# Kernel tuning notes

Hardware: AMD Instinct MI355X
Metric: run time of the kernel (lower is better)

Reference implementation:

```python
import jax, jax.numpy as jnp
import numpy as np

DIM = 256; HEADS = 8; HD = DIM // HEADS; WIN = 3; LOCAL = WIN * WIN
SR = 8; SHARED = 4; ROUTED = 2
B = 4; RES = 64; TBL = 4096
EPS = 1.1920929e-07  # torch.finfo(float32).eps


def _l2(x):
    return x / jnp.clip(jnp.linalg.norm(x, axis=-1, keepdims=True), EPS)


def _forward(x, relative_coords_table, q_w, q_b, kv_w, kv_b, temperature,
             query_embedding, rpb_local, learnable_tokens, learnable_bias,
             cpb1_w, cpb1_b, cpb2_w, cpb2_b, sr_w, sr_b, norm_g, norm_b,
             wg_w, wg0_w, wg1_w, proj_w, proj_b, relative_pos_index, H, W):
    B_, N, C = x.shape
    pH, pW = H // SR, W // SR
    PL = pH * pW
    _x = x.reshape(B_ * N, C)

    # ---- MoE head routing: top-k gating over routed heads ----
    gates = jax.nn.softmax(_x @ wg_w.T, axis=1)                 # (BN, n_routed)
    _, idx = jax.lax.top_k(gates, ROUTED)
    mask = jax.nn.one_hot(idx, gates.shape[1], dtype=gates.dtype).sum(axis=1)
    rg = gates * mask
    rg = rg / jnp.clip(jnp.sum(rg, axis=1, keepdims=True), EPS)
    routed_gates = rg.reshape(B_, N, -1) * ROUTED

    # ---- seq-length-scale buffer: log(local valid-window count + pool_len) ----
    r = WIN // 2
    ch = np.minimum(np.arange(H) + r, H - 1) - np.maximum(np.arange(H) - r, 0) + 1
    cw = np.minimum(np.arange(W) + r, W - 1) - np.maximum(np.arange(W) - r, 0) + 1
    sls = jnp.asarray(np.log(np.outer(ch, cw).reshape(-1, 1).astype(np.float32) + PL))

    # ---- queries ----
    q = (x @ q_w.T + q_b).reshape(B_, N, HEADS, HD).transpose(0, 2, 1, 3)
    q_norm = _l2(q)                                             # (B,h,N,d)
    q_scaled = (q_norm + query_embedding) * jax.nn.softplus(temperature) * sls

    # ---- local branch: unfold normalized k and v over 3x3 windows (zero pad) ----
    kv = x @ kv_w.T + kv_b                                      # (B,N,2C)
    k_loc = _l2(kv[..., :C].reshape(B_, N, HEADS, HD)).reshape(B_, N, C)
    kvl = jnp.concatenate([k_loc, kv[..., C:]], -1).transpose(0, 2, 1).reshape(B_, 2 * C, H, W)
    kvp = jnp.pad(kvl, ((0, 0), (0, 0), (r, r), (r, r)))
    patches = jnp.stack([kvp[:, :, i:i + H, j:j + W] for i in range(WIN) for j in range(WIN)], axis=2)
    patches = patches.reshape(B_, 2 * HEADS, HD, LOCAL, N).transpose(0, 1, 4, 2, 3)  # (B,2h,N,d,L)
    k_local, v_local = patches[:, :HEADS], patches[:, HEADS:]

    attn_local = jnp.einsum('bhnd,bhndl->bhnl', q_scaled, k_local) + rpb_local[:, None, :]

    # ---- pooled global branch ----
    x_ = x.transpose(0, 2, 1).reshape(B_, C, H, W)
    x_ = jnp.einsum('oc,bchw->bohw', sr_w, x_) + sr_b[None, :, None, None]  # 1x1 conv
    x_ = jax.nn.gelu(x_, approximate=False)
    x_ = x_.reshape(B_, C, pH, SR, pW, SR).mean((3, 5)).reshape(B_, C, PL).transpose(0, 2, 1)
    mu = x_.mean(-1, keepdims=True)
    var = ((x_ - mu) ** 2).mean(-1, keepdims=True)
    x_ = (x_ - mu) / jnp.sqrt(var + 1e-5) * norm_g + norm_b
    kvp2 = (x_ @ kv_w.T + kv_b).reshape(B_, PL, 2 * HEADS, HD).transpose(0, 2, 1, 3)
    k_pool, v_pool = kvp2[:, :HEADS], kvp2[:, HEADS:]

    cpb = jax.nn.relu(relative_coords_table @ cpb1_w.T + cpb1_b) @ cpb2_w.T + cpb2_b  # (T,h)
    pool_bias = cpb.T[:, relative_pos_index.reshape(-1)].reshape(HEADS, N, PL)
    attn_pool = jnp.einsum('bhnd,bhpd->bhnp', q_scaled, _l2(k_pool)) + pool_bias

    # ---- joint softmax over local + pooled keys ----
    attn = jax.nn.softmax(jnp.concatenate([attn_local, attn_pool], axis=-1), axis=-1)
    a_loc, a_pool = attn[..., :LOCAL], attn[..., LOCAL:]
    a_loc = jnp.einsum('bhnd,hdl->bhnl', q_norm, learnable_tokens) + learnable_bias + a_loc
    x_local = jnp.einsum('bhnl,bhndl->bhnd', a_loc, v_local)
    x_pool = jnp.einsum('bhnp,bhpd->bhnd', a_pool, v_pool)
    out = (x_local + x_pool).transpose(0, 2, 1, 3)              # (B,N,h,d)

    # ---- combine shared + routed head gates ----
    shared_gates = jax.nn.softmax(_x @ wg1_w.T, axis=1).reshape(B_, N, SHARED) * SHARED
    w0 = jax.nn.softmax(_x @ wg0_w.T, axis=1).reshape(B_, N, 2) * 2
    masked = jnp.concatenate([w0[..., 0:1] * shared_gates, w0[..., 1:2] * routed_gates], axis=-1)
    out = (masked[..., None] * out).reshape(B_, N, C)
    return out @ proj_w.T + proj_b


def setup_inputs() -> dict:
    key = jax.random.key(0)
    ks = jax.random.split(key, 20)
    H = W = RES
    N = H * W
    C = DIM
    PL = (H // SR) * (W // SR)

    def nrm(i, shape, s=0.02):
        return jax.random.normal(ks[i], shape, dtype=jnp.float32) * s

    return {
        'x': jax.random.normal(ks[0], (B, N, C), dtype=jnp.float32),
        'relative_coords_table': jax.random.normal(ks[1], (TBL, 2), dtype=jnp.float32),
        'q_w': nrm(3, (C, C)), 'q_b': jnp.zeros((C,), jnp.float32),
        'kv_w': nrm(4, (2 * C, C)), 'kv_b': jnp.zeros((2 * C,), jnp.float32),
        'temperature': jnp.full((HEADS, 1, 1), float(np.log(np.exp(1 / 0.24) - 1)), jnp.float32),
        'query_embedding': nrm(5, (HEADS, 1, HD)),
        'rpb_local': nrm(6, (HEADS, LOCAL), 0.0004),
        'learnable_tokens': nrm(7, (HEADS, HD, LOCAL)),
        'learnable_bias': jnp.zeros((HEADS, 1, LOCAL), jnp.float32),
        'cpb1_w': nrm(8, (512, 2)), 'cpb1_b': jnp.zeros((512,), jnp.float32),
        'cpb2_w': nrm(9, (HEADS, 512)), 'cpb2_b': jnp.zeros((HEADS,), jnp.float32),
        'sr_w': nrm(10, (C, C)), 'sr_b': jnp.zeros((C,), jnp.float32),
        'norm_g': jnp.ones((C,), jnp.float32), 'norm_b': jnp.zeros((C,), jnp.float32),
        'wg_w': nrm(11, (HEADS - SHARED, C)),
        'wg0_w': nrm(12, (2, C)),
        'wg1_w': nrm(13, (SHARED, C)),
        'proj_w': nrm(14, (C, C)), 'proj_b': jnp.zeros((C,), jnp.float32),
        'relative_pos_index': jax.random.randint(ks[2], (N, PL), 0, TBL, dtype=jnp.int32),
        'H': H, 'W': W,
    }


def reference(x, relative_coords_table, q_w, q_b, kv_w, kv_b, temperature,
              query_embedding, rpb_local, learnable_tokens, learnable_bias,
              cpb1_w, cpb1_b, cpb2_w, cpb2_b, sr_w, sr_b, norm_g, norm_b,
              wg_w, wg0_w, wg1_w, proj_w, proj_b, relative_pos_index, H, W):
    return _forward(x, relative_coords_table, q_w, q_b, kv_w, kv_b, temperature,
                    query_embedding, rpb_local, learnable_tokens, learnable_bias,
                    cpb1_w, cpb1_b, cpb2_w, cpb2_b, sr_w, sr_b, norm_g, norm_b,
                    wg_w, wg0_w, wg1_w, proj_w, proj_b, relative_pos_index, H, W)
```

## Files before the change

kernel.cpp:

```cpp
#include <hip/hip_runtime.h>
#include <math.h>

#define EPSF 1.1920929e-07f

typedef __attribute__((ext_vector_type(8))) short short8;
typedef __attribute__((ext_vector_type(4))) float f32x4;

static __device__ __forceinline__ unsigned short f2bf(float f) {
    unsigned int u = __float_as_uint(f);
    return (unsigned short)((u + 0x7FFFu + ((u >> 16) & 1u)) >> 16);
}
static __device__ __forceinline__ float bf2f(unsigned short u) {
    return __uint_as_float((unsigned int)u << 16);
}

__global__ __launch_bounds__(256) void convert_x(
    const float* __restrict__ x, unsigned short* __restrict__ xbf)
{
    const int e = (blockIdx.x * 256 + threadIdx.x) * 4;
    float4 v = *(const float4*)(x + e);
    ushort4 o;
    o.x = f2bf(v.x); o.y = f2bf(v.y); o.z = f2bf(v.z); o.w = f2bf(v.w);
    *(ushort4*)(xbf + e) = o;
}

__global__ __launch_bounds__(256) void convert_w(
    const float* __restrict__ q_w, const float* __restrict__ kv_w,
    const float* __restrict__ sr_w, const float* __restrict__ pw,
    unsigned short* __restrict__ wcat, unsigned short* __restrict__ pwbf)
{
    const int e = (blockIdx.x * 256 + threadIdx.x) * 4;
    if (e < 262144) {
        int n = e >> 8, k = e & 255;
        const float* src = (n < 256) ? (q_w + n*256) :
                           (n < 768) ? (kv_w + (n-256)*256) : (sr_w + (n-768)*256);
        float4 v = *(const float4*)(src + k);
        ushort4 o;
        o.x = f2bf(v.x); o.y = f2bf(v.y); o.z = f2bf(v.z); o.w = f2bf(v.w);
        *(ushort4*)(wcat + e) = o;
    } else {
        int e2 = e - 262144;
        float4 v = *(const float4*)(pw + e2);
        ushort4 o;
        o.x = f2bf(v.x); o.y = f2bf(v.y); o.z = f2bf(v.z); o.w = f2bf(v.w);
        *(ushort4*)(pwbf + e2) = o;
    }
}

__global__ __launch_bounds__(256) void gemm_mfma(
    const unsigned short* __restrict__ A,
    const unsigned short* __restrict__ W,
    const float* __restrict__ B0, const float* __restrict__ B1,
    const float* __restrict__ B2,
    int r1, int r2, int mode,
    float* __restrict__ C, int ldc,
    unsigned short* __restrict__ qkv,
    const float* __restrict__ temp, const float* __restrict__ qe)
{
    __shared__ __attribute__((aligned(16))) unsigned short At[64*264];
    __shared__ __attribute__((aligned(16))) unsigned short Bt[64*264];
    const int m0 = blockIdx.y << 6;
    const int n0 = blockIdx.x << 6;
    const int t  = threadIdx.x;
    const int w  = t >> 6;
    const int col16 = t & 15;
    const int quad  = (t & 63) >> 4;

    const float* Bp; int noff;
    if (n0 < r1)      { Bp = B0; noff = 0;  }
    else if (n0 < r2) { Bp = B1; noff = r1; }
    else              { Bp = B2; noff = r2; }

    uint4 av[8], bv[8];
#pragma unroll
    for (int j = 0; j < 8; ++j) {
        int ci = j*256 + t;
        int r = ci >> 5, c = ci & 31;
        av[j] = *(const uint4*)(A + (size_t)(m0 + r)*256 + c*8);
        bv[j] = *(const uint4*)(W + (size_t)(n0 + r)*256 + c*8);
    }
#pragma unroll
    for (int j = 0; j < 8; ++j) {
        int ci = j*256 + t;
        int r = ci >> 5, c = ci & 31;
        *(uint4*)(At + r*264 + c*8) = av[j];
        *(uint4*)(Bt + r*264 + c*8) = bv[j];
    }
    __syncthreads();

    f32x4 acc[4];
#pragma unroll
    for (int ct = 0; ct < 4; ++ct) acc[ct] = (f32x4){0.f, 0.f, 0.f, 0.f};
#pragma unroll
    for (int kk = 0; kk < 8; ++kk) {
        short8 af = *(const short8*)(At + (w*16 + col16)*264 + kk*32 + quad*8);
#pragma unroll
        for (int ct = 0; ct < 4; ++ct) {
            short8 bf = *(const short8*)(Bt + (ct*16 + col16)*264 + kk*32 + quad*8);
            acc[ct] = __builtin_amdgcn_mfma_f32_16x16x32_bf16(af, bf, acc[ct], 0, 0, 0);
        }
    }

    float bias_c[4];
#pragma unroll
    for (int ct = 0; ct < 4; ++ct)
        bias_c[ct] = Bp[n0 + ct*16 + col16 - noff];

    if (mode == 0) {
        const int region = n0 >> 8;
        float qe_c[4], spt_c[4];
        if (region == 0) {
#pragma unroll
            for (int c = 0; c < 4; ++c) {
                int col = n0 + c*16 + col16;
                spt_c[c] = log1pf(expf(temp[(col >> 5) & 7]));
                qe_c[c]  = qe[col];
            }
        }
#pragma unroll
        for (int reg = 0; reg < 4; ++reg) {
            const int row = m0 + w*16 + quad*4 + reg;
            float v[4];
#pragma unroll
            for (int c = 0; c < 4; ++c) v[c] = acc[c][reg] + bias_c[c];
            if (region <= 1) {
#pragma unroll
                for (int hp = 0; hp < 2; ++hp) {
                    float s = v[2*hp]*v[2*hp] + v[2*hp+1]*v[2*hp+1];
                    s += __shfl_xor(s, 1); s += __shfl_xor(s, 2);
                    s += __shfl_xor(s, 4); s += __shfl_xor(s, 8);
                    float inv = 1.0f / fmaxf(sqrtf(s), EPSF);
                    v[2*hp]   *= inv;
                    v[2*hp+1] *= inv;
                }
            }
            if (region == 0) {
                int n = row & 4095;
                int y = n >> 6, x = n & 63;
                int cy = (y == 0 || y == 63) ? 2 : 3;
                int cx = (x == 0 || x == 63) ? 2 : 3;
                float sls = logf((float)(cy*cx) + 64.0f);
#pragma unroll
                for (int c = 0; c < 4; ++c)
                    v[c] = (v[c] + qe_c[c]) * (spt_c[c] * sls);
            }
            if (region == 3) {
#pragma unroll
                for (int c = 0; c < 4; ++c) {
                    float g = 0.5f * v[c] * (1.0f + erff(v[c] * 0.70710678118654752f));
                    C[(size_t)row * ldc + n0 + c*16 + col16] = g;
                }
            } else {
#pragma unroll
                for (int c = 0; c < 4; ++c)
                    qkv[(size_t)row * 2048 + n0 + c*16 + col16] = f2bf(v[c]);
            }
        }
    } else {
#pragma unroll
        for (int reg = 0; reg < 4; ++reg) {
            const int row = m0 + w*16 + quad*4 + reg;
#pragma unroll
            for (int c = 0; c < 4; ++c)
                C[(size_t)row * ldc + n0 + c*16 + col16] = acc[c][reg] + bias_c[c];
        }
    }
}

__global__ __launch_bounds__(256) void gate_kernel(
    const float* __restrict__ x,
    const float* __restrict__ wg,
    const float* __restrict__ wg0,
    const float* __restrict__ wg1,
    float* __restrict__ gate)
{
    __shared__ float wsm[10*272];
    const int t  = threadIdx.x;
    const int t0 = blockIdx.x << 6;
    for (int i = t; i < 2560; i += 256) {
        int f = i >> 8, k = i & 255;
        const float* src = (f < 4) ? (wg + f*256) : (f < 6) ? (wg0 + (f-4)*256) : (wg1 + (f-6)*256);
        wsm[f*272 + (k & 63) + (k >> 6)*68] = src[k];
    }
    __syncthreads();
    const int tok = t >> 2, sub = t & 3;
    const float4* xr = (const float4*)(x + (size_t)(t0 + tok)*256 + sub*64);
    float4 xv[16];
#pragma unroll
    for (int i = 0; i < 16; ++i) xv[i] = xr[i];
    float d[10];
#pragma unroll
    for (int f = 0; f < 10; ++f) {
        const float* wrow = wsm + f*272 + sub*68;
        float s = 0.f;
#pragma unroll
        for (int i = 0; i < 16; ++i) {
            float4 wv = *(const float4*)(wrow + i*4);
            s += xv[i].x*wv.x + xv[i].y*wv.y + xv[i].z*wv.z + xv[i].w*wv.w;
        }
        s += __shfl_xor(s, 1, 4);
        s += __shfl_xor(s, 2, 4);
        d[f] = s;
    }
    if (sub == 0) {
        float e[4];
        float m = fmaxf(fmaxf(d[0],d[1]), fmaxf(d[2],d[3]));
        float ssum = 0.f;
        for (int i = 0; i < 4; ++i) { e[i] = expf(d[i]-m); ssum += e[i]; }
        for (int i = 0; i < 4; ++i) e[i] /= ssum;
        int i1 = 0;
        for (int i = 1; i < 4; ++i) if (e[i] > e[i1]) i1 = i;
        int i2 = -1;
        for (int i = 0; i < 4; ++i) if (i != i1 && (i2 < 0 || e[i] > e[i2])) i2 = i;
        float rs = fmaxf(e[i1] + e[i2], EPSF);
        float rg[4] = {0.f,0.f,0.f,0.f};
        rg[i1] = e[i1] / rs * 2.f;
        rg[i2] = e[i2] / rs * 2.f;
        float sh[4];
        float m1 = fmaxf(fmaxf(d[6],d[7]), fmaxf(d[8],d[9]));
        float s1 = 0.f;
        for (int i = 0; i < 4; ++i) { sh[i] = expf(d[6+i]-m1); s1 += sh[i]; }
        float mm = fmaxf(d[4], d[5]);
        float e0 = expf(d[4]-mm), e1 = expf(d[5]-mm);
        float w00 = e0/(e0+e1)*2.f, w01 = e1/(e0+e1)*2.f;
        float* gr = gate + ((size_t)(t0 + tok) << 3);
        for (int i = 0; i < 4; ++i) gr[i]   = w00 * (sh[i]/s1*4.f);
        for (int i = 0; i < 4; ++i) gr[4+i] = w01 * rg[i];
    }
}

__global__ __launch_bounds__(256) void pool_ln_kernel(
    const float* __restrict__ buf,
    const float* __restrict__ g, const float* __restrict__ bb,
    float* __restrict__ xp)
{
    __shared__ float r1[256], r2[256];
    const int blk = blockIdx.x;
    const int b = blk >> 6, p = blk & 63;
    const int py = p >> 3, px = p & 7;
    const int t = threadIdx.x;
    float acc = 0.f;
    for (int dy = 0; dy < 8; ++dy)
#pragma unroll
        for (int dx = 0; dx < 8; ++dx) {
            int s = ((py*8+dy) << 6) + px*8 + dx;
            acc += buf[(((size_t)(b*4096+s)) << 10) + 768 + t];
        }
    acc *= (1.0f/64.0f);
    r1[t] = acc; r2[t] = acc*acc;
    __syncthreads();
    for (int off = 128; off; off >>= 1) {
        if (t < off) { r1[t] += r1[t+off]; r2[t] += r2[t+off]; }
        __syncthreads();
    }
    float mu  = r1[0] * (1.0f/256.0f);
    float var = r2[0] * (1.0f/256.0f) - mu*mu;
    float rstd = rsqrtf(var + 1e-5f);
    xp[((size_t)blk << 8) + t] = (acc - mu) * rstd * g[t] + bb[t];
}

__global__ __launch_bounds__(256) void kvpool_kernel(
    const float* __restrict__ xp,
    const float* __restrict__ kv_w, const float* __restrict__ kv_b,
    unsigned short* __restrict__ kpb, unsigned short* __restrict__ vpb)
{
    __shared__ float xs[256];
    __shared__ float row[512];
    __shared__ float inv[8];
    const int blk = blockIdx.x;
    const int t = threadIdx.x;
    xs[t] = xp[((size_t)blk << 8) + t];
    __syncthreads();
    for (int o = t; o < 512; o += 256) {
        const float* wr = kv_w + ((size_t)o << 8);
        float s = kv_b[o];
        for (int k = 0; k < 256; ++k) s += xs[k]*wr[k];
        row[o] = s;
    }
    __syncthreads();
    if (t < 8) {
        float s = 0.f;
        for (int dd = 0; dd < 32; ++dd) { float v = row[t*32+dd]; s += v*v; }
        inv[t] = 1.0f / fmaxf(sqrtf(s), EPSF);
    }
    __syncthreads();
    const int b = blk >> 6, p = blk & 63, h = t >> 5, dd = t & 31;
    size_t o = ((((size_t)(b*8+h))*64 + p) << 5) + dd;
    kpb[o] = f2bf(row[t] * inv[h]);
    vpb[o] = f2bf(row[256 + t]);
}

__global__ __launch_bounds__(256) void cpb_kernel(
    const float* __restrict__ tbl,
    const float* __restrict__ w1, const float* __restrict__ b1,
    const float* __restrict__ w2, const float* __restrict__ b2,
    float* __restrict__ cpb)
{
    __shared__ float hid[512];
    const int r = blockIdx.x, t = threadIdx.x;
    const float c0 = tbl[(size_t)r*2], c1 = tbl[(size_t)r*2+1];
    for (int i = t; i < 512; i += 256)
        hid[i] = fmaxf(c0*w1[i*2] + c1*w1[i*2+1] + b1[i], 0.f);
    __syncthreads();
    const int h = t >> 5, dd = t & 31;
    float s = 0.f;
    for (int i = dd; i < 512; i += 32) s += hid[i] * w2[h*512+i];
    for (int off = 16; off; off >>= 1) s += __shfl_xor(s, off, 32);
    if (dd == 0) cpb[((size_t)r << 3) + h] = s + b2[h];
}

__global__ __launch_bounds__(256, 4) void attn_mfma(
    const unsigned short* __restrict__ qkv,
    unsigned short* __restrict__ ao,
    const unsigned short* __restrict__ kpb,
    const unsigned short* __restrict__ vpb,
    const float* __restrict__ cpb,
    const int*   __restrict__ rpi,
    const float* __restrict__ temp,
    const float* __restrict__ qe,
    const float* __restrict__ rpb,
    const float* __restrict__ lt,
    const float* __restrict__ lb,
    const float* __restrict__ gate)
{
    __shared__ __attribute__((aligned(16))) unsigned short U0[112*40];
    __shared__ __attribute__((aligned(16))) unsigned short U1[64*40];
    __shared__ __attribute__((aligned(16))) unsigned short QS[64*40];
    __shared__ __attribute__((aligned(16))) unsigned short P[64*136];
    __shared__ __attribute__((aligned(16))) unsigned short LTT[16*40];
    __shared__ float invscL[64], gateL[64], rpbL[9], dqvL[16];

    const int tile = blockIdx.x;
    const int h    = blockIdx.y;
    const int b    = blockIdx.z;
    const int ty0  = (tile >> 3) << 3;
    const int tx0  = (tile & 7) << 3;
    const int t    = threadIdx.x;

    const float spt = log1pf(expf(temp[h]));
    if (t < 64) {
        int y = ty0 + (t >> 3), x = tx0 + (t & 7);
        int cy = (y == 0 || y == 63) ? 2 : 3;
        int cx = (x == 0 || x == 63) ? 2 : 3;
        invscL[t] = 1.0f / (spt * logf((float)(cy*cx) + 64.0f));
        gateL[t] = gate[(((size_t)(b*4096 + ((y<<6)|x))) << 3) + h];
    } else if (t < 80) {
        int j = t - 64;
        float s = 0.f;
        if (j < 9) {
            s = lb[h*9 + j];
            for (int dd = 0; dd < 32; ++dd)
                s -= qe[h*32+dd] * lt[(h*32+dd)*9 + j];
        }
        dqvL[j] = s;
    } else if (t < 89) {
        rpbL[t-80] = rpb[h*9 + (t-80)];
    }
    for (int i = t; i < 16*32; i += 256) {
        int j = i >> 5, dd = i & 31;
        LTT[j*40 + dd] = (j < 9) ? f2bf(lt[(h*32+dd)*9 + j]) : (unsigned short)0;
    }

    unsigned short* KH = U0;
    unsigned short* KP = U1;
    for (int i = t; i < 112*8; i += 256) {
        int r = i >> 3, sg = i & 7;
        uint2 val = {0u, 0u};
        if (r < 100) {
            int y = ty0 + r/10 - 1, x = tx0 + r%10 - 1;
            if (y >= 0 && y < 64 && x >= 0 && x < 64)
                val = *(const uint2*)(qkv + (size_t)(b*4096 + ((y<<6)|x))*2048 + 256 + h*32 + sg*4);
        }
        *(uint2*)(KH + r*40 + sg*4) = val;
    }
    {
        const unsigned short* src = kpb + (size_t)(b*8+h)*2048;
        for (int i = t; i < 512; i += 256)
            *(uint2*)(KP + (i >> 3)*40 + (i & 7)*4) = *(const uint2*)(src + i*4);
    }
    for (int i = t; i < 512; i += 256) {
        int n = i >> 3, sg = i & 7;
        int y = ty0 + (n >> 3), x = tx0 + (n & 7);
        *(uint2*)(QS + n*40 + sg*4) =
            *(const uint2*)(qkv + (size_t)(b*4096 + ((y<<6)|x))*2048 + h*32 + sg*4);
    }
    __syncthreads();

    const int lane  = t & 63;
    const int w     = t >> 6;
    const int col16 = lane & 15;
    const int quad  = lane >> 4;
    const int s_w   = (20*w) & ~15;

    float pbias[4][4];
#pragma unroll
    for (int ct = 0; ct < 4; ++ct) {
        int p = ct*16 + col16;
#pragma unroll
        for (int reg = 0; reg < 4; ++reg) {
            int n = w*16 + quad*4 + reg;
            int y = ty0 + (n >> 3), x = tx0 + (n & 7);
            int ngl = (y << 6) | x;
            pbias[ct][reg] = cpb[((size_t)rpi[(size_t)ngl*64 + p] << 3) + h];
        }
    }

    short8 aq = *(const short8*)(QS + (w*16 + col16)*40 + quad*8);
    f32x4 cl[4], cp[4];
    {
        const f32x4 z = {0.f, 0.f, 0.f, 0.f};
#pragma unroll
        for (int ct = 0; ct < 4; ++ct) {
            short8 bk = *(const short8*)(KH + (s_w + ct*16 + col16)*40 + quad*8);
            cl[ct] = __builtin_amdgcn_mfma_f32_16x16x32_bf16(aq, bk, z, 0, 0, 0);
        }
#pragma unroll
        for (int ct = 0; ct < 4; ++ct) {
            short8 bp = *(const short8*)(KP + (ct*16 + col16)*40 + quad*8);
            cp[ct] = __builtin_amdgcn_mfma_f32_16x16x32_bf16(aq, bp, z, 0, 0, 0);
        }
    }
#pragma unroll
    for (int ct = 0; ct < 4; ++ct) {
        int hk = s_w + ct*16 + col16;
        int ky = hk / 10, kx = hk - ky*10;
#pragma unroll
        for (int reg = 0; reg < 4; ++reg) {
            int n = w*16 + quad*4 + reg;
            int dy = ky - (n >> 3), dx = kx - (n & 7);
            bool valid = (dy >= 0 && dy <= 2 && dx >= 0 && dx <= 2);
            cl[ct][reg] = valid ? (cl[ct][reg] + rpbL[dy*3 + dx]) : -1e30f;
        }
    }
#pragma unroll
    for (int ct = 0; ct < 4; ++ct)
#pragma unroll
        for (int reg = 0; reg < 4; ++reg)
            cp[ct][reg] += pbias[ct][reg];
    float inv[4];
#pragma unroll
    for (int reg = 0; reg < 4; ++reg) {
        float m = -1e30f;
#pragma unroll
        for (int ct = 0; ct < 4; ++ct) m = fmaxf(m, cl[ct][reg]);
#pragma unroll
        for (int ct = 0; ct < 4; ++ct) m = fmaxf(m, cp[ct][reg]);
        m = fmaxf(m, __shfl_xor(m, 1)); m = fmaxf(m, __shfl_xor(m, 2));
        m = fmaxf(m, __shfl_xor(m, 4)); m = fmaxf(m, __shfl_xor(m, 8));
        float s = 0.f;
#pragma unroll
        for (int ct = 0; ct < 4; ++ct) {
            float e = __builtin_expf(cl[ct][reg] - m); cl[ct][reg] = e; s += e;
        }
#pragma unroll
        for (int ct = 0; ct < 4; ++ct) {
            float e = __builtin_expf(cp[ct][reg] - m); cp[ct][reg] = e; s += e;
        }
        s += __shfl_xor(s, 1); s += __shfl_xor(s, 2);
        s += __shfl_xor(s, 4); s += __shfl_xor(s, 8);
        inv[reg] = 1.0f / s;
    }
#pragma unroll
    for (int ct = 0; ct < 4; ++ct)
#pragma unroll
        for (int reg = 0; reg < 4; ++reg) {
            int n = w*16 + quad*4 + reg;
            P[n*136 + ct*16 + col16] = f2bf(cl[ct][reg] * inv[reg]);
        }
#pragma unroll
    for (int ct = 0; ct < 4; ++ct)
#pragma unroll
        for (int reg = 0; reg < 4; ++reg) {
            int n = w*16 + quad*4 + reg;
            P[n*136 + 64 + ct*16 + col16] = f2bf(cp[ct][reg] * inv[reg]);
        }
    {
        const f32x4 z = {0.f, 0.f, 0.f, 0.f};
        short8 blt = *(const short8*)(LTT + col16*40 + quad*8);
        f32x4 cd = __builtin_amdgcn_mfma_f32_16x16x32_bf16(aq, blt, z, 0, 0, 0);
        if (col16 < 9) {
            int dy = col16 / 3, dx = col16 - dy*3;
#pragma unroll
            for (int reg = 0; reg < 4; ++reg) {
                int n = w*16 + quad*4 + reg;
                float ltv = cd[reg] * invscL[n] + dqvL[col16];
                int hk = ((n >> 3) + dy)*10 + (n & 7) + dx;
                int pc = hk - s_w;
                P[n*136 + pc] = f2bf(bf2f(P[n*136 + pc]) + ltv);
            }
        }
    }
    __syncthreads();

    unsigned short* VT  = U0;
    unsigned short* VPT = U1;
    for (int i = t; i < 1792; i += 256) {
        int rlo = i & 15, rest = i >> 4;
        int dp = rest & 15, r = (rest >> 4)*16 + rlo;
        unsigned val = 0;
        if (r < 100) {
            int y = ty0 + r/10 - 1, x = tx0 + r%10 - 1;
            if (y >= 0 && y < 64 && x >= 0 && x < 64)
                val = *(const unsigned*)(qkv + (size_t)(b*4096 + ((y<<6)|x))*2048 + 512 + h*32 + dp*2);
        }
        VT[(2*dp)*136 + r]   = (unsigned short)(val & 0xffffu);
        VT[(2*dp+1)*136 + r] = (unsigned short)(val >> 16);
    }
    for (int i = t; i < 1024; i += 256) {
        int plo = i & 15, rest = i >> 4;
        int dp = rest & 15, p = (rest >> 4)*16 + plo;
        unsigned val = *(const unsigned*)(vpb + (size_t)(b*8+h)*2048 + p*32 + dp*2);
        VPT[(2*dp)*72 + p]   = (unsigned short)(val & 0xffffu);
        VPT[(2*dp+1)*72 + p] = (unsigned short)(val >> 16);
    }
    __syncthreads();

    f32x4 o0 = {0.f,0.f,0.f,0.f}, o1 = {0.f,0.f,0.f,0.f};
#pragma unroll
    for (int ks = 0; ks < 4; ++ks) {
        short8 a = *(const short8*)(P + (w*16 + col16)*136 + ks*32 + quad*8);
        short8 b0, b1;
        if (ks < 2) {
            b0 = *(const short8*)(VT + col16*136      + s_w + ks*32 + quad*8);
            b1 = *(const short8*)(VT + (16+col16)*136 + s_w + ks*32 + quad*8);
        } else {
            b0 = *(const short8*)(VPT + col16*72      + (ks-2)*32 + quad*8);
            b1 = *(const short8*)(VPT + (16+col16)*72 + (ks-2)*32 + quad*8);
        }
        o0 = __builtin_amdgcn_mfma_f32_16x16x32_bf16(a, b0, o0, 0, 0, 0);
        o1 = __builtin_amdgcn_mfma_f32_16x16x32_bf16(a, b1, o1, 0, 0, 0);
    }
#pragma unroll
    for (int reg = 0; reg < 4; ++reg) {
        int n = w*16 + quad*4 + reg;
        int y = ty0 + (n >> 3), x = tx0 + (n & 7);
        size_t rowo = (size_t)(b*4096 + ((y<<6)|x))*256 + h*32;
        float g = gateL[n];
        ao[rowo + col16]      = f2bf(o0[reg] * g);
        ao[rowo + 16 + col16] = f2bf(o1[reg] * g);
    }
}

extern "C" void kernel_launch(void* const* d_in, const int* in_sizes, int n_in,
                              void* d_out, int out_size, void* d_ws, size_t ws_size,
                              hipStream_t stream)
{
    const float* x    = (const float*)d_in[0];
    const float* tbl  = (const float*)d_in[1];
    const float* q_w  = (const float*)d_in[2];
    const float* q_b  = (const float*)d_in[3];
    const float* kv_w = (const float*)d_in[4];
    const float* kv_b = (const float*)d_in[5];
    const float* temp = (const float*)d_in[6];
    const float* qe   = (const float*)d_in[7];
    const float* rpb  = (const float*)d_in[8];
    const float* lt   = (const float*)d_in[9];
    const float* lb   = (const float*)d_in[10];
    const float* c1w  = (const float*)d_in[11];
    const float* c1b  = (const float*)d_in[12];
    const float* c2w  = (const float*)d_in[13];
    const float* c2b  = (const float*)d_in[14];
    const float* sr_w = (const float*)d_in[15];
    const float* sr_b = (const float*)d_in[16];
    const float* ng   = (const float*)d_in[17];
    const float* nbias= (const float*)d_in[18];
    const float* wg   = (const float*)d_in[19];
    const float* wg0  = (const float*)d_in[20];
    const float* wg1  = (const float*)d_in[21];
    const float* pw   = (const float*)d_in[22];
    const float* pb   = (const float*)d_in[23];
    const int*   rpi  = (const int*)d_in[24];
    (void)in_sizes; (void)n_in; (void)out_size; (void)ws_size;

    float* buf   = (float*)d_ws;
    unsigned short* qkvb = (unsigned short*)d_ws;
    float* xp    = buf + (size_t)16384*1024;
    float* kpoolf= xp + 65536;
    unsigned short* kpb = (unsigned short*)kpoolf;
    unsigned short* vpb = kpb + 131072;
    float* cpbb  = kpoolf + 131072;
    float* gateb = cpbb + 32768;
    unsigned short* xbf  = (unsigned short*)(gateb + 131072);
    unsigned short* ao   = xbf;
    unsigned short* wcat = xbf + (size_t)16384*256;
    unsigned short* pwbf = wcat + 262144;
    float* out   = (float*)d_out;

    convert_x<<<4096,256,0,stream>>>(x, xbf);
    convert_w<<<320,256,0,stream>>>(q_w, kv_w, sr_w, pw, wcat, pwbf);
    gemm_mfma<<<dim3(16,256),256,0,stream>>>(xbf, wcat, q_b, kv_b, sr_b,
                                             256, 768, 0, buf, 1024,
                                             qkvb, temp, qe);
    gate_kernel<<<256,256,0,stream>>>(x, wg, wg0, wg1, gateb);
    pool_ln_kernel<<<256,256,0,stream>>>(buf, ng, nbias, xp);
    kvpool_kernel<<<256,256,0,stream>>>(xp, kv_w, kv_b, kpb, vpb);
    cpb_kernel<<<4096,256,0,stream>>>(tbl, c1w, c1b, c2w, c2b, cpbb);
    attn_mfma<<<dim3(64,8,4),256,0,stream>>>(qkvb, ao, kpb, vpb, cpbb, rpi,
                                             temp, qe, rpb, lt, lb, gateb);
    gemm_mfma<<<dim3(4,256),256,0,stream>>>(ao, pwbf, pb, pb, pb,
                                            1<<30, 1<<30, 1, out, 256,
                                            (unsigned short*)nullptr, nullptr, nullptr);
}
```

Baseline: 267.6 us.

## Fuse prep kernels, merge pool-LN with KV projection, precompute halo offsets

Merges the x/weight bf16 conversion, gating computation and CPB MLP into one prep kernel, and merges pool+LayerNorm with the pooled KV projection. This cuts the launch count from nine to five and lets the gate reuse x already loaded for conversion, removing a second read of x. In attention, per-row halo global offsets are precomputed once into shared memory instead of recomputing the bounds checks per load, at the cost of an extra barrier. The fused prep kernel's blocks take divergent branches and use a shared buffer only some of them need.

```diff
diff --git a/kernel.cpp b/kernel.cpp
--- a/kernel.cpp
+++ b/kernel.cpp
@@ -14,36 +14,93 @@
     return __uint_as_float((unsigned int)u << 16);
 }
 
-__global__ __launch_bounds__(256) void convert_x(
-    const float* __restrict__ x, unsigned short* __restrict__ xbf)
-{
-    const int e = (blockIdx.x * 256 + threadIdx.x) * 4;
-    float4 v = *(const float4*)(x + e);
-    ushort4 o;
-    o.x = f2bf(v.x); o.y = f2bf(v.y); o.z = f2bf(v.z); o.w = f2bf(v.w);
-    *(ushort4*)(xbf + e) = o;
-}
-
-__global__ __launch_bounds__(256) void convert_w(
+__global__ __launch_bounds__(256) void prep_kernel(
+    const float* __restrict__ x,
+    const float* __restrict__ wg,  const float* __restrict__ wg0,
+    const float* __restrict__ wg1,
     const float* __restrict__ q_w, const float* __restrict__ kv_w,
     const float* __restrict__ sr_w, const float* __restrict__ pw,
-    unsigned short* __restrict__ wcat, unsigned short* __restrict__ pwbf)
+    const float* __restrict__ tbl,
+    const float* __restrict__ c1w, const float* __restrict__ c1b,
+    const float* __restrict__ c2w, const float* __restrict__ c2b,
+    unsigned short* __restrict__ xbf, float* __restrict__ gate,
+    unsigned short* __restrict__ wcat, unsigned short* __restrict__ pwbf,
+    float* __restrict__ cpb)
 {
-    const int e = (blockIdx.x * 256 + threadIdx.x) * 4;
-    if (e < 262144) {
-        int n = e >> 8, k = e & 255;
-        const float* src = (n < 256) ? (q_w + n*256) :
-                           (n < 768) ? (kv_w + (n-256)*256) : (sr_w + (n-768)*256);
-        float4 v = *(const float4*)(src + k);
+    __shared__ float shpad[512];
+    const int blk = blockIdx.x;
+    const int t   = threadIdx.x;
+    if (blk < 4096) {
+        const int j = t & 63;
+        const int row = (blk << 2) + (t >> 6);
+        float4 v = *(const float4*)(x + (size_t)row*256 + j*4);
         ushort4 o;
         o.x = f2bf(v.x); o.y = f2bf(v.y); o.z = f2bf(v.z); o.w = f2bf(v.w);
-        *(ushort4*)(wcat + e) = o;
+        *(ushort4*)(xbf + (size_t)row*256 + j*4) = o;
+        float d[10];
+#pragma unroll
+        for (int f = 0; f < 10; ++f) {
+            const float* wf = (f < 4) ? (wg + f*256) : (f < 6) ? (wg0 + (f-4)*256)
+                                                               : (wg1 + (f-6)*256);
+            float4 wv = *(const float4*)(wf + j*4);
+            float s = v.x*wv.x + v.y*wv.y + v.z*wv.z + v.w*wv.w;
+            s += __shfl_xor(s, 32); s += __shfl_xor(s, 16); s += __shfl_xor(s, 8);
+            s += __shfl_xor(s, 4);  s += __shfl_xor(s, 2);  s += __shfl_xor(s, 1);
+            d[f] = s;
+        }
+        if (j == 0) {
+            float e[4];
+            float m = fmaxf(fmaxf(d[0],d[1]), fmaxf(d[2],d[3]));
+            float ssum = 0.f;
+            for (int i = 0; i < 4; ++i) { e[i] = expf(d[i]-m); ssum += e[i]; }
+            for (int i = 0; i < 4; ++i) e[i] /= ssum;
+            int i1 = 0;
+            for (int i = 1; i < 4; ++i) if (e[i] > e[i1]) i1 = i;
+            int i2 = -1;
+            for (int i = 0; i < 4; ++i) if (i != i1 && (i2 < 0 || e[i] > e[i2])) i2 = i;
+            float rs = fmaxf(e[i1] + e[i2], EPSF);
+            float rg[4] = {0.f,0.f,0.f,0.f};
+            rg[i1] = e[i1] / rs * 2.f;
+            rg[i2] = e[i2] / rs * 2.f;
+            float sh[4];
+            float m1 = fmaxf(fmaxf(d[6],d[7]), fmaxf(d[8],d[9]));
+            float s1 = 0.f;
+            for (int i = 0; i < 4; ++i) { sh[i] = expf(d[6+i]-m1); s1 += sh[i]; }
+            float mm = fmaxf(d[4], d[5]);
+            float e0 = expf(d[4]-mm), e1 = expf(d[5]-mm);
+            float w00 = e0/(e0+e1)*2.f, w01 = e1/(e0+e1)*2.f;
+            float* gr = gate + ((size_t)row << 3);
+            for (int i = 0; i < 4; ++i) gr[i]   = w00 * (sh[i]/s1*4.f);
+            for (int i = 0; i < 4; ++i) gr[4+i] = w01 * rg[i];
+        }
+    } else if (blk < 4416) {
+        const int e = ((blk - 4096)*256 + t)*4;
+        if (e < 262144) {
+            int n = e >> 8, k = e & 255;
+            const float* src = (n < 256) ? (q_w + n*256) :
+                               (n < 768) ? (kv_w + (n-256)*256) : (sr_w + (n-768)*256);
+            float4 v = *(const float4*)(src + k);
+            ushort4 o;
+            o.x = f2bf(v.x); o.y = f2bf(v.y); o.z = f2bf(v.z); o.w = f2bf(v.w);
+            *(ushort4*)(wcat + e) = o;
+        } else {
+            int e2 = e - 262144;
+            float4 v = *(const float4*)(pw + e2);
+            ushort4 o;
+            o.x = f2bf(v.x); o.y = f2bf(v.y); o.z = f2bf(v.z); o.w = f2bf(v.w);
+            *(ushort4*)(pwbf + e2) = o;
+        }
     } else {
-        int e2 = e - 262144;
-        float4 v = *(const float4*)(pw + e2);
-        ushort4 o;
-        o.x = f2bf(v.x); o.y = f2bf(v.y); o.z = f2bf(v.z); o.w = f2bf(v.w);
-        *(ushort4*)(pwbf + e2) = o;
+        const int r = blk - 4416;
+        const float c0 = tbl[(size_t)r*2], c1 = tbl[(size_t)r*2+1];
+        for (int i = t; i < 512; i += 256)
+            shpad[i] = fmaxf(c0*c1w[i*2] + c1*c1w[i*2+1] + c1b[i], 0.f);
+        __syncthreads();
+        const int hh = t >> 5, dd = t & 31;
+        float s = 0.f;
+        for (int i = dd; i < 512; i += 32) s += shpad[i] * c2w[hh*512+i];
+        for (int off = 16; off; off >>= 1) s += __shfl_xor(s, off, 32);
+        if (dd == 0) cpb[((size_t)r << 3) + hh] = s + c2b[hh];
     }
 }
 
@@ -167,74 +224,16 @@
     }
 }
 
-__global__ __launch_bounds__(256) void gate_kernel(
-    const float* __restrict__ x,
-    const float* __restrict__ wg,
-    const float* __restrict__ wg0,
-    const float* __restrict__ wg1,
-    float* __restrict__ gate)
-{
-    __shared__ float wsm[10*272];
-    const int t  = threadIdx.x;
-    const int t0 = blockIdx.x << 6;
-    for (int i = t; i < 2560; i += 256) {
-        int f = i >> 8, k = i & 255;
-        const float* src = (f < 4) ? (wg + f*256) : (f < 6) ? (wg0 + (f-4)*256) : (wg1 + (f-6)*256);
-        wsm[f*272 + (k & 63) + (k >> 6)*68] = src[k];
-    }
-    __syncthreads();
-    const int tok = t >> 2, sub = t & 3;
-    const float4* xr = (const float4*)(x + (size_t)(t0 + tok)*256 + sub*64);
-    float4 xv[16];
-#pragma unroll
-    for (int i = 0; i < 16; ++i) xv[i] = xr[i];
-    float d[10];
-#pragma unroll
-    for (int f = 0; f < 10; ++f) {
-        const float* wrow = wsm + f*272 + sub*68;
-        float s = 0.f;
-#pragma unroll
-        for (int i = 0; i < 16; ++i) {
-            float4 wv = *(const float4*)(wrow + i*4);
-            s += xv[i].x*wv.x + xv[i].y*wv.y + xv[i].z*wv.z + xv[i].w*wv.w;
-        }
-        s += __shfl_xor(s, 1, 4);
-        s += __shfl_xor(s, 2, 4);
-        d[f] = s;
-    }
-    if (sub == 0) {
-        float e[4];
-        float m = fmaxf(fmaxf(d[0],d[1]), fmaxf(d[2],d[3]));
-        float ssum = 0.f;
-        for (int i = 0; i < 4; ++i) { e[i] = expf(d[i]-m); ssum += e[i]; }
-        for (int i = 0; i < 4; ++i) e[i] /= ssum;
-        int i1 = 0;
-        for (int i = 1; i < 4; ++i) if (e[i] > e[i1]) i1 = i;
-        int i2 = -1;
-        for (int i = 0; i < 4; ++i) if (i != i1 && (i2 < 0 || e[i] > e[i2])) i2 = i;
-        float rs = fmaxf(e[i1] + e[i2], EPSF);
-        float rg[4] = {0.f,0.f,0.f,0.f};
-        rg[i1] = e[i1] / rs * 2.f;
-        rg[i2] = e[i2] / rs * 2.f;
-        float sh[4];
-        float m1 = fmaxf(fmaxf(d[6],d[7]), fmaxf(d[8],d[9]));
-        float s1 = 0.f;
-        for (int i = 0; i < 4; ++i) { sh[i] = expf(d[6+i]-m1); s1 += sh[i]; }
-        float mm = fmaxf(d[4], d[5]);
-        float e0 = expf(d[4]-mm), e1 = expf(d[5]-mm);
-        float w00 = e0/(e0+e1)*2.f, w01 = e1/(e0+e1)*2.f;
-        float* gr = gate + ((size_t)(t0 + tok) << 3);
-        for (int i = 0; i < 4; ++i) gr[i]   = w00 * (sh[i]/s1*4.f);
-        for (int i = 0; i < 4; ++i) gr[4+i] = w01 * rg[i];
-    }
-}
-
-__global__ __launch_bounds__(256) void pool_ln_kernel(
+__global__ __launch_bounds__(256) void poolkv_kernel(
     const float* __restrict__ buf,
     const float* __restrict__ g, const float* __restrict__ bb,
-    float* __restrict__ xp)
+    const float* __restrict__ kv_w, const float* __restrict__ kv_b,
+    unsigned short* __restrict__ kpb, unsigned short* __restrict__ vpb)
 {
     __shared__ float r1[256], r2[256];
+    __shared__ float xs[256];
+    __shared__ float rowv[512];
+    __shared__ float inv[8];
     const int blk = blockIdx.x;
     const int b = blk >> 6, p = blk & 63;
     const int py = p >> 3, px = p & 7;
@@ -256,57 +255,25 @@
     float mu  = r1[0] * (1.0f/256.0f);
     float var = r2[0] * (1.0f/256.0f) - mu*mu;
     float rstd = rsqrtf(var + 1e-5f);
-    xp[((size_t)blk << 8) + t] = (acc - mu) * rstd * g[t] + bb[t];
-}
-
-__global__ __launch_bounds__(256) void kvpool_kernel(
-    const float* __restrict__ xp,
-    const float* __restrict__ kv_w, const float* __restrict__ kv_b,
-    unsigned short* __restrict__ kpb, unsigned short* __restrict__ vpb)
-{
-    __shared__ float xs[256];
-    __shared__ float row[512];
-    __shared__ float inv[8];
-    const int blk = blockIdx.x;
-    const int t = threadIdx.x;
-    xs[t] = xp[((size_t)blk << 8) + t];
+    xs[t] = (acc - mu) * rstd * g[t] + bb[t];
     __syncthreads();
     for (int o = t; o < 512; o += 256) {
         const float* wr = kv_w + ((size_t)o << 8);
         float s = kv_b[o];
         for (int k = 0; k < 256; ++k) s += xs[k]*wr[k];
-        row[o] = s;
+        rowv[o] = s;
     }
     __syncthreads();
     if (t < 8) {
         float s = 0.f;
-        for (int dd = 0; dd < 32; ++dd) { float v = row[t*32+dd]; s += v*v; }
+        for (int dd = 0; dd < 32; ++dd) { float v = rowv[t*32+dd]; s += v*v; }
         inv[t] = 1.0f / fmaxf(sqrtf(s), EPSF);
     }
     __syncthreads();
-    const int b = blk >> 6, p = blk & 63, h = t >> 5, dd = t & 31;
-    size_t o = ((((size_t)(b*8+h))*64 + p) << 5) + dd;
-    kpb[o] = f2bf(row[t] * inv[h]);
-    vpb[o] = f2bf(row[256 + t]);
-}
-
-__global__ __launch_bounds__(256) void cpb_kernel(
-    const float* __restrict__ tbl,
-    const float* __restrict__ w1, const float* __restrict__ b1,
-    const float* __restrict__ w2, const float* __restrict__ b2,
-    float* __restrict__ cpb)
-{
-    __shared__ float hid[512];
-    const int r = blockIdx.x, t = threadIdx.x;
-    const float c0 = tbl[(size_t)r*2], c1 = tbl[(size_t)r*2+1];
-    for (int i = t; i < 512; i += 256)
-        hid[i] = fmaxf(c0*w1[i*2] + c1*w1[i*2+1] + b1[i], 0.f);
-    __syncthreads();
-    const int h = t >> 5, dd = t & 31;
-    float s = 0.f;
-    for (int i = dd; i < 512; i += 32) s += hid[i] * w2[h*512+i];
-    for (int off = 16; off; off >>= 1) s += __shfl_xor(s, off, 32);
-    if (dd == 0) cpb[((size_t)r << 3) + h] = s + b2[h];
+    const int h = t >> 5;
+    size_t o = ((((size_t)(b*8+h))*64 + p) << 5) + (t & 31);
+    kpb[o] = f2bf(rowv[t] * inv[h]);
+    vpb[o] = f2bf(rowv[256 + t]);
 }
 
 __global__ __launch_bounds__(256, 4) void attn_mfma(
@@ -329,6 +296,7 @@
     __shared__ __attribute__((aligned(16))) unsigned short P[64*136];
     __shared__ __attribute__((aligned(16))) unsigned short LTT[16*40];
     __shared__ float invscL[64], gateL[64], rpbL[9], dqvL[16];
+    __shared__ int hofs[112];
 
     const int tile = blockIdx.x;
     const int h    = blockIdx.y;
@@ -355,22 +323,31 @@
         dqvL[j] = s;
     } else if (t < 89) {
         rpbL[t-80] = rpb[h*9 + (t-80)];
+    } else if (t >= 128 && t < 240) {
+        int r = t - 128;
+        int off = -1;
+        if (r < 100) {
+            int y = ty0 + r/10 - 1, x = tx0 + r%10 - 1;
+            if (y >= 0 && y < 64 && x >= 0 && x < 64)
+                off = (b*4096 + ((y<<6)|x))*2048 + h*32;
+        }
+        hofs[r] = off;
+        if (r >= 100) hofs[r] = -1;
     }
     for (int i = t; i < 16*32; i += 256) {
         int j = i >> 5, dd = i & 31;
         LTT[j*40 + dd] = (j < 9) ? f2bf(lt[(h*32+dd)*9 + j]) : (unsigned short)0;
     }
+    __syncthreads();
 
     unsigned short* KH = U0;
     unsigned short* KP = U1;
     for (int i = t; i < 112*8; i += 256) {
         int r = i >> 3, sg = i & 7;
+        int off = hofs[r];
         uint2 val = {0u, 0u};
-        if (r < 100) {
-            int y = ty0 + r/10 - 1, x = tx0 + r%10 - 1;
-            if (y >= 0 && y < 64 && x >= 0 && x < 64)
-                val = *(const uint2*)(qkv + (size_t)(b*4096 + ((y<<6)|x))*2048 + 256 + h*32 + sg*4);
-        }
+        if (off >= 0)
+            val = *(const uint2*)(qkv + (size_t)off + 256 + sg*4);
         *(uint2*)(KH + r*40 + sg*4) = val;
     }
     {
@@ -380,9 +357,8 @@
     }
     for (int i = t; i < 512; i += 256) {
         int n = i >> 3, sg = i & 7;
-        int y = ty0 + (n >> 3), x = tx0 + (n & 7);
-        *(uint2*)(QS + n*40 + sg*4) =
-            *(const uint2*)(qkv + (size_t)(b*4096 + ((y<<6)|x))*2048 + h*32 + sg*4);
+        int off = hofs[(n >> 3)*10 + (n & 7) + 11];
+        *(uint2*)(QS + n*40 + sg*4) = *(const uint2*)(qkv + (size_t)off + sg*4);
     }
     __syncthreads();
 
@@ -497,12 +473,10 @@
     for (int i = t; i < 1792; i += 256) {
         int rlo = i & 15, rest = i >> 4;
         int dp = rest & 15, r = (rest >> 4)*16 + rlo;
+        int off = hofs[r];
         unsigned val = 0;
-        if (r < 100) {
-            int y = ty0 + r/10 - 1, x = tx0 + r%10 - 1;
-            if (y >= 0 && y < 64 && x >= 0 && x < 64)
-                val = *(const unsigned*)(qkv + (size_t)(b*4096 + ((y<<6)|x))*2048 + 512 + h*32 + dp*2);
-        }
+        if (off >= 0)
+            val = *(const unsigned*)(qkv + (size_t)off + 512 + dp*2);
         VT[(2*dp)*136 + r]   = (unsigned short)(val & 0xffffu);
         VT[(2*dp+1)*136 + r] = (unsigned short)(val >> 16);
     }
@@ -586,15 +560,13 @@
     unsigned short* pwbf = wcat + 262144;
     float* out   = (float*)d_out;
 
-    convert_x<<<4096,256,0,stream>>>(x, xbf);
-    convert_w<<<320,256,0,stream>>>(q_w, kv_w, sr_w, pw, wcat, pwbf);
+    prep_kernel<<<8512,256,0,stream>>>(x, wg, wg0, wg1, q_w, kv_w, sr_w, pw,
+                                       tbl, c1w, c1b, c2w, c2b,
+                                       xbf, gateb, wcat, pwbf, cpbb);
     gemm_mfma<<<dim3(16,256),256,0,stream>>>(xbf, wcat, q_b, kv_b, sr_b,
                                              256, 768, 0, buf, 1024,
                                              qkvb, temp, qe);
-    gate_kernel<<<256,256,0,stream>>>(x, wg, wg0, wg1, gateb);
-    pool_ln_kernel<<<256,256,0,stream>>>(buf, ng, nbias, xp);
-    kvpool_kernel<<<256,256,0,stream>>>(xp, kv_w, kv_b, kpb, vpb);
-    cpb_kernel<<<4096,256,0,stream>>>(tbl, c1w, c1b, c2w, c2b, cpbb);
+    poolkv_kernel<<<256,256,0,stream>>>(buf, ng, nbias, kv_w, kv_b, kpb, vpb);
     attn_mfma<<<dim3(64,8,4),256,0,stream>>>(qkvb, ao, kpb, vpb, cpbb, rpi,
                                              temp, qe, rpb, lt, lb, gateb);
     gemm_mfma<<<dim3(4,256),256,0,stream>>>(ao, pwbf, pb, pb, pb,
```

Result: faster. 260.3 us (-2.7%).
